# Kernel tuning notes

Measured on AMD Instinct MI355X. Metric: run time of the kernel, lower is better.

Reference implementation:

```python
import jax, jax.numpy as jnp
from jax import lax
import numpy as np

NUM_BLOCK, NUM_LAYER = 4, 10
DILATIONS = [2 ** (i % NUM_LAYER) for i in range(NUM_BLOCK * NUM_LAYER)]


def setup_inputs() -> dict:
    key = jax.random.key(0)
    ks = jax.random.split(key, 6)
    s = 0.05
    return {
        "x": jax.random.normal(ks[0], (8, 256, 16000), dtype=jnp.float32),
        "W_start": jax.random.normal(ks[1], (32, 256), dtype=jnp.float32) * s,
        "W_dil": jax.random.normal(ks[2], (40, 128, 32, 2), dtype=jnp.float32) * s,
        "W_res": jax.random.normal(ks[3], (40, 32, 128), dtype=jnp.float32) * s,
        "W_e1": jax.random.normal(ks[4], (256, 32), dtype=jnp.float32) * s,
        "W_e2": jax.random.normal(ks[5], (256, 256), dtype=jnp.float32) * s,
    }


def _causal_dilated_conv(x, w, dilation):
    # x: [B, Cin, T], w: [Cout, Cin, K=2]. Left-pad (K-1)*dilation -> causal,
    # equivalent to torch symmetric-pad-then-trim-right.
    pad = (w.shape[-1] - 1) * dilation
    return lax.conv_general_dilated(
        x, w, window_strides=(1,), padding=[(pad, 0)],
        rhs_dilation=(dilation,), dimension_numbers=("NCH", "OIH", "NCH"))


def reference(x, W_start, W_dil, W_res, W_e1, W_e2):
    # start 1x1 conv (no bias)
    residual = jnp.einsum("oc,bct->bot", W_start, x)  # [B,32,T]
    skips = jnp.zeros_like(residual)
    for i, d in enumerate(DILATIONS):
        h = _causal_dilated_conv(residual, W_dil[i], d)       # [B,128,T]
        g = jnp.tanh(h) * jax.nn.sigmoid(h)                   # gated activation
        skip = jnp.einsum("oc,bct->bot", W_res[i], g)         # 1x1 -> [B,32,T]
        residual = residual + skip
        skips = skips + skip
    h = jax.nn.relu(skips)
    h = jax.nn.relu(jnp.einsum("oc,bct->bot", W_e1, h))       # [B,256,T]
    logits = jnp.einsum("oc,bct->bot", W_e2, h)               # [B,256,T]
    return logits
```

## Files before the change

### kernel.cpp

```cpp
#include <hip/hip_runtime.h>
#include <math.h>

#define T_LEN 16000
#define NTILE 250
#define TT 64
#define NBLK 2000
#define LGRID 500

static const int N_RES = 8 * 32 * T_LEN;

typedef _Float16 half_t;
typedef __attribute__((ext_vector_type(8))) _Float16 halfx8;
typedef __attribute__((ext_vector_type(4))) _Float16 halfx4;
typedef __attribute__((ext_vector_type(16))) float f32x16;
typedef unsigned int uint32;
typedef unsigned short ushort16;

#define MFMA(a, b, c) __builtin_amdgcn_mfma_f32_32x32x16_f16((a), (b), (c), 0, 0, 0)

static __device__ inline uint32 packpair(float a, float b) {
  half_t ha = (half_t)a, hb = (half_t)b;
  return (uint32)__builtin_bit_cast(ushort16, ha) |
         ((uint32)__builtin_bit_cast(ushort16, hb) << 16);
}

__global__ __launch_bounds__(256) void repack_k(
    const float* __restrict__ Wd, const float* __restrict__ Wr,
    const float* __restrict__ Ws, const float* __restrict__ We1,
    const float* __restrict__ We2,
    half_t* __restrict__ WaG, half_t* __restrict__ WrG, float* __restrict__ WsT,
    half_t* __restrict__ We1S, half_t* __restrict__ We2S) {
  int i = blockIdx.x * 256 + threadIdx.x;
  if (i < 40 * 128 * 128) {
    int l = i >> 14, r = i & 16383, o = r >> 7, k = r & 127;
    int kk = k & 63, c = kk >> 1, s = kk & 1;
    float w = Wd[(((l * 128 + o) * 32 + c) << 1) + s];
    half_t w0 = (half_t)w;
    WaG[i] = (k < 64) ? w0 : (half_t)((w - (float)w0) * 2048.f);
  }
  if (i < 40 * 32 * 256) {
    int l = i >> 13, r = i & 8191, o2 = r >> 8, k = r & 255;
    int kk = k & 127;
    int ks = kk >> 4, lh = (kk >> 3) & 1, j = kk & 7;
    int mh = ks >> 2, til = (ks >> 1) & 1, ab = ks & 1;
    int m = mh * 64 + til * 32 + ab * 16 + (j & 3) + ((j >> 2) << 3) + lh * 4;
    float w = Wr[(l * 32 + o2) * 128 + m];
    half_t w0 = (half_t)w;
    WrG[i] = (k < 128) ? w0 : (half_t)((w - (float)w0) * 2048.f);
  }
  if (i < 8192) {
    int c = i >> 5, o = i & 31;
    WsT[i] = Ws[o * 256 + c];
  }
  if (i < 16384) {
    int o = i >> 6, k = i & 63;
    float w = We1[o * 32 + (k & 31)];
    half_t w0 = (half_t)w;
    We1S[i] = (k < 32) ? w0 : (half_t)((w - (float)w0) * 2048.f);
  }
  if (i < 131072) {
    int o = i >> 9, k = i & 511;
    float w = We2[o * 256 + (k & 255)];
    half_t w0 = (half_t)w;
    We2S[i] = (k < 256) ? w0 : (half_t)((w - (float)w0) * 2048.f);
  }
}

__global__ __launch_bounds__(256) void start_k(const float* __restrict__ x,
                                               const float* __restrict__ WsT,
                                               float* __restrict__ res) {
  __shared__ float xs[32][68];
  int b = blockIdx.x / NTILE;
  int t0 = (blockIdx.x % NTILE) * TT;
  int tid = threadIdx.x;
  int o = tid & 31, tg = (tid >> 5) * 8;
  int lr = tid >> 3, lt = (tid & 7) * 8;
  float acc[8];
#pragma unroll
  for (int j = 0; j < 8; ++j) acc[j] = 0.f;
  for (int cc = 0; cc < 8; ++cc) {
    __syncthreads();
    const float* xp = x + ((size_t)b * 256 + cc * 32 + lr) * T_LEN + t0 + lt;
    *(float4*)&xs[lr][lt]     = *(const float4*)xp;
    *(float4*)&xs[lr][lt + 4] = *(const float4*)(xp + 4);
    __syncthreads();
#pragma unroll 4
    for (int c = 0; c < 32; ++c) {
      float w = WsT[(cc * 32 + c) * 32 + o];
      const float* xr = &xs[c][tg];
#pragma unroll
      for (int j = 0; j < 8; ++j) acc[j] += w * xr[j];
    }
  }
  float* rp = res + ((size_t)b * 32 + o) * T_LEN + t0 + tg;
  *(float4*)rp       = make_float4(acc[0], acc[1], acc[2], acc[3]);
  *(float4*)(rp + 4) = make_float4(acc[4], acc[5], acc[6], acc[7]);
}

#define LOAD_TILE(TI, CV, PV)                                              \
  {                                                                        \
    int tl_ = blockIdx.x + (TI) * LGRID;                                   \
    int bb_ = tl_ / NTILE;                                                 \
    int tb_ = (tl_ - bb_ * NTILE) * TT;                                    \
    const float* rip_ = resIn + ((size_t)bb_ * 32 + cth) * T_LEN;          \
    *(float4*)(CV)       = *(const float4*)(rip_ + tb_ + twh);             \
    *(float4*)((CV) + 4) = *(const float4*)(rip_ + tb_ + twh + 4);         \
    int tp_ = tb_ + twh - d;                                               \
    if (tp_ >= 0 && (d & 3) == 0) {                                        \
      *(float4*)(PV)       = *(const float4*)(rip_ + tp_);                 \
      *(float4*)((PV) + 4) = *(const float4*)(rip_ + tp_ + 4);             \
    } else {                                                               \
      _Pragma("unroll")                                                    \
      for (int j_ = 0; j_ < 8; ++j_) {                                     \
        int q_ = tp_ + j_;                                                 \
        (PV)[j_] = (q_ >= 0) ? rip_[q_] : 0.f;                             \
      }                                                                    \
    }                                                                      \
  }

#define TILE_BODY(TI, CV, PV, NCV, NPV, PREF)                                  \
  {                                                                            \
    int tile = blockIdx.x + (TI) * LGRID;                                      \
    int b = tile / NTILE;                                                      \
    int t0 = (tile - b * NTILE) * TT;                                          \
                                             \
    _Pragma("unroll")                                                          \
    for (int j = 0; j < 8; ++j) {                                              \
      int t = twh + j;                                                         \
      int sw = ((t >> 3) & 3) << 5;                                            \
      char* zrow = sm + t * 272;                                               \
      half_t p0 = (half_t)(PV)[j];                                             \
      half_t c0 = (half_t)(CV)[j];                                             \
      float pl = ((PV)[j] - (float)p0) * 2048.f;                               \
      float cl = ((CV)[j] - (float)c0) * 2048.f;                               \
      *(uint32*)(zrow + ((cth * 4) ^ sw))       = packpair((PV)[j], (CV)[j]);  \
      *(uint32*)(zrow + ((cth * 4 + 128) ^ sw)) = packpair(pl, cl);            \
    }                                                                          \
    __syncthreads();                                                           \
       \
    if (PREF) { LOAD_TILE((TI) + 1, NCV, NPV); }                               \
                                      \
    f32x16 hi0{}, hi1{}, lo0{}, lo1{};                                         \
    {                                                                          \
      int colt = nh * 32 + l31;                                                \
      int sw = ((colt >> 3) & 3) << 5;                                         \
      const char* zr = sm + colt * 272;                                        \
      _Pragma("unroll")                                                        \
      for (int ks = 0; ks < 12; ++ks) {                                        \
        int brow = (ks < 4) ? ks * 16                                          \
                            : ((ks < 8) ? (ks & 3) * 16 + 64 : (ks & 3) * 16); \
        halfx8 bf = *(const halfx8*)(zr + ((brow * 2 + lhi * 16) ^ sw));       \
        if (ks < 4) {                                                          \
          hi0 = MFMA(a1h0[ks], bf, hi0);                                       \
          hi1 = MFMA(a1h1[ks], bf, hi1);                                       \
        } else if (ks < 8) {                                                   \
          lo0 = MFMA(a1h0[ks & 3], bf, lo0);                                   \
          lo1 = MFMA(a1h1[ks & 3], bf, lo1);                                   \
        } else {                                                               \
          lo0 = MFMA(a1l0[ks & 3], bf, lo0);                                   \
          lo1 = MFMA(a1l1[ks & 3], bf, lo1);                                   \
        }                                                                      \
      }                                                                        \
    }                                                                          \
                          \
    halfx8 gh0a, gh0b, gl0a, gl0b, gh1a, gh1b, gl1a, gl1b;                     \
    _Pragma("unroll")                                                          \
    for (int r = 0; r < 16; ++r) {                                             \
      float ha = hi0[r] + lo0[r] * (1.f / 2048.f);                             \
      float hb = hi1[r] + lo1[r] * (1.f / 2048.f);                             \
      ha = fmaxf(ha, -30.f);                                                   \
      hb = fmaxf(hb, -30.f);                                                   \
      float ea = __expf(-ha), eb = __expf(-hb);                                \
      float ga = (1.f - ea) * __builtin_amdgcn_rcpf(1.f + ea * ea);            \
      float gb = (1.f - eb) * __builtin_amdgcn_rcpf(1.f + eb * eb);            \
      half_t ga0 = (half_t)ga;                                                 \
      half_t gb0 = (half_t)gb;                                                 \
      half_t ga1 = (half_t)((ga - (float)ga0) * 2048.f);                       \
      half_t gb1 = (half_t)((gb - (float)gb0) * 2048.f);                       \
      if (r < 8) {                                                             \
        gh0a[r] = ga0; gl0a[r] = ga1; gh1a[r] = gb0; gl1a[r] = gb1;            \
      } else {                                                                 \
        gh0b[r - 8] = ga0; gl0b[r - 8] = ga1;                                  \
        gh1b[r - 8] = gb0; gl1b[r - 8] = gb1;                                  \
      }                                                                        \
    }                                                                          \
                         \
    f32x16 shi{}, slo{};                                                       \
    shi = MFMA(wrHi[0], gh0a, shi);                                            \
    shi = MFMA(wrHi[1], gh0b, shi);                                            \
    shi = MFMA(wrHi[2], gh1a, shi);                                            \
    shi = MFMA(wrHi[3], gh1b, shi);                                            \
    slo = MFMA(wrHi[0], gl0a, slo);                                            \
    slo = MFMA(wrHi[1], gl0b, slo);                                            \
    slo = MFMA(wrHi[2], gl1a, slo);                                            \
    slo = MFMA(wrHi[3], gl1b, slo);                                            \
    slo = MFMA(wrLo[0], gh0a, slo);                                            \
    slo = MFMA(wrLo[1], gh0b, slo);                                            \
    slo = MFMA(wrLo[2], gh1a, slo);                                            \
    slo = MFMA(wrLo[3], gh1b, slo);                                            \
    __syncthreads();                      \
    {                                                                          \
      float* skb = (float*)sm + mh * 32 * 68;                                  \
      _Pragma("unroll")                                                        \
      for (int r = 0; r < 16; ++r) {                                           \
        int row = (r & 3) + 8 * (r >> 2) + 4 * lhi;                            \
        skb[row * 68 + nh * 32 + l31] = shi[r] + slo[r] * (1.f / 2048.f);      \
      }                                                                        \
    }                                                                          \
    __syncthreads();                                                           \
                     \
    {                                                                          \
      const float* s0 = (const float*)sm + cth * 68 + twh;                     \
      const float* s1 = s0 + 32 * 68;                                          \
      size_t base = ((size_t)b * 32 + cth) * T_LEN + t0 + twh;                 \
      _Pragma("unroll")                                                        \
      for (int v = 0; v < 8; v += 4) {                                         \
        float4 sa = *(const float4*)(s0 + v);                                  \
        float4 sb = *(const float4*)(s1 + v);                                  \
        float4 o;                                                              \
        o.x = (CV)[v]     + sa.x + sb.x;                                       \
        o.y = (CV)[v + 1] + sa.y + sb.y;                                       \
        o.z = (CV)[v + 2] + sa.z + sb.z;                                       \
        o.w = (CV)[v + 3] + sa.w + sb.w;                                       \
        *(float4*)(resOut + base + v) = o;                                     \
      }                                                                        \
    }                                                                          \
    __syncthreads();       \
  }

__global__ __launch_bounds__(256, 2) void layer_k(const float* __restrict__ resIn,
                                                  float* __restrict__ resOut,
                                                  const half_t* __restrict__ WaL,
                                                  const half_t* __restrict__ WrL,
                                                  int d) {
  __shared__ __align__(16) char sm[17408];
  int tid = threadIdx.x;
  int wave = tid >> 6, lane = tid & 63;
  int l31 = lane & 31, lhi = lane >> 5;
  int mh = wave & 1, nh = wave >> 1;
  int cth = tid >> 3, twh = (tid & 7) * 8;

  halfx8 a1h0[4], a1l0[4], a1h1[4], a1l1[4];
  {
    const half_t* wa = WaL + (mh * 64 + l31) * 128 + lhi * 8;
#pragma unroll
    for (int j = 0; j < 4; ++j) {
      a1h0[j] = *(const halfx8*)(wa + j * 16);
      a1l0[j] = *(const halfx8*)(wa + 64 + j * 16);
      a1h1[j] = *(const halfx8*)(wa + 32 * 128 + j * 16);
      a1l1[j] = *(const halfx8*)(wa + 32 * 128 + 64 + j * 16);
    }
  }
  halfx8 wrHi[4], wrLo[4];
  {
    const half_t* wr = WrL + l31 * 256 + mh * 64 + lhi * 8;
#pragma unroll
    for (int q = 0; q < 4; ++q) {
      wrHi[q] = *(const halfx8*)(wr + q * 16);
      wrLo[q] = *(const halfx8*)(wr + 128 + q * 16);
    }
  }

  float cvA[8], pvA[8], cvB[8], pvB[8];
  LOAD_TILE(0, cvA, pvA);

  TILE_BODY(0, cvA, pvA, cvB, pvB, 1)
  TILE_BODY(1, cvB, pvB, cvA, pvA, 1)
  TILE_BODY(2, cvA, pvA, cvB, pvB, 1)
  TILE_BODY(3, cvB, pvB, cvA, pvA, 0)
}

__global__ __launch_bounds__(512) void end_k(const float* __restrict__ resF,
                                             const float* __restrict__ res0,
                                             const half_t* __restrict__ We1S,
                                             const half_t* __restrict__ We2S,
                                             float* __restrict__ out) {
  __shared__ __align__(16) char sm[75776];
  const int H2T_OFF = 0, H1F_OFF = 0, H1T_OFF = 66560;
  int tid = threadIdx.x;
  int b = blockIdx.x / NTILE;
  int t0 = (blockIdx.x % NTILE) * TT;

  {
    int c = tid >> 4, tt4 = (tid & 15) * 4;
    size_t base = ((size_t)b * 32 + c) * T_LEN + t0 + tt4;
    float4 f = *(const float4*)(resF + base);
    float4 z = *(const float4*)(res0 + base);
    float* h1 = (float*)(sm + H1F_OFF) + c * 68 + tt4;
    h1[0] = fmaxf(f.x - z.x, 0.f);
    h1[1] = fmaxf(f.y - z.y, 0.f);
    h1[2] = fmaxf(f.z - z.z, 0.f);
    h1[3] = fmaxf(f.w - z.w, 0.f);
  }
  __syncthreads();
  {
    int t = tid & 63, cg2 = tid >> 6;
    const float* h1 = (const float*)(sm + H1F_OFF);
    halfx4 hi, lo;
#pragma unroll
    for (int j = 0; j < 4; ++j) {
      float v = h1[(cg2 * 4 + j) * 68 + t];
      half_t h = (half_t)v;
      hi[j] = h;
      lo[j] = (half_t)((v - (float)h) * 2048.f);
    }
    half_t* h1t = (half_t*)(sm + H1T_OFF) + t * 72;
    *(halfx4*)(h1t + cg2 * 4)      = hi;
    *(halfx4*)(h1t + 32 + cg2 * 4) = lo;
  }
  __syncthreads();

  int wave = tid >> 6, lane = tid & 63;
  int l31 = lane & 31, lhi = lane >> 5;

  f32x16 aHi0{}, aHi1{}, aLo0{}, aLo1{};
  {
    const char* h1t = sm + H1T_OFF;
    const half_t* wp = We1S + (wave * 32 + l31) * 64;
#pragma unroll
    for (int ks = 0; ks < 2; ++ks) {
      halfx8 hiA = *(const halfx8*)(wp + ks * 16 + lhi * 8);
      halfx8 loA = *(const halfx8*)(wp + 32 + ks * 16 + lhi * 8);
      const char* br0 = h1t + l31 * 144;
      const char* br1 = h1t + (32 + l31) * 144;
      halfx8 hiB0 = *(const halfx8*)(br0 + (ks * 16 + lhi * 8) * 2);
      halfx8 loB0 = *(const halfx8*)(br0 + (32 + ks * 16 + lhi * 8) * 2);
      halfx8 hiB1 = *(const halfx8*)(br1 + (ks * 16 + lhi * 8) * 2);
      halfx8 loB1 = *(const halfx8*)(br1 + (32 + ks * 16 + lhi * 8) * 2);
      aHi0 = MFMA(hiA, hiB0, aHi0);
      aLo0 = MFMA(hiA, loB0, aLo0);
      aLo0 = MFMA(loA, hiB0, aLo0);
      aHi1 = MFMA(hiA, hiB1, aHi1);
      aLo1 = MFMA(hiA, loB1, aLo1);
      aLo1 = MFMA(loA, hiB1, aLo1);
    }
  }
  {
#pragma unroll
    for (int n = 0; n < 2; ++n) {
      const f32x16& aH = n ? aHi1 : aHi0;
      const f32x16& aL = n ? aLo1 : aLo0;
      int t = n * 32 + l31;
      half_t* row = (half_t*)(sm + H2T_OFF) + t * 520;
#pragma unroll
      for (int g = 0; g < 4; ++g) {
        halfx4 hi, lo;
#pragma unroll
        for (int j = 0; j < 4; ++j) {
          int r = g * 4 + j;
          float v = aH[r] + aL[r] * (1.f / 2048.f);
          v = fmaxf(v, 0.f);
          half_t h = (half_t)v;
          hi[j] = h;
          lo[j] = (half_t)((v - (float)h) * 2048.f);
        }
        int col = wave * 32 + g * 8 + lhi * 4;
        *(halfx4*)(row + col)       = hi;
        *(halfx4*)(row + 256 + col) = lo;
      }
    }
  }
  __syncthreads();

  f32x16 bHi0{}, bHi1{}, bLo0{}, bLo1{};
  {
    const half_t* wp = We2S + (size_t)(wave * 32 + l31) * 512;
    const char* h2t = sm + H2T_OFF;
#pragma unroll 2
    for (int ks = 0; ks < 16; ++ks) {
      halfx8 hiA = *(const halfx8*)(wp + ks * 16 + lhi * 8);
      halfx8 loA = *(const halfx8*)(wp + 256 + ks * 16 + lhi * 8);
      const char* br0 = h2t + l31 * 1040;
      const char* br1 = h2t + (32 + l31) * 1040;
      halfx8 hiB0 = *(const halfx8*)(br0 + (ks * 16 + lhi * 8) * 2);
      halfx8 loB0 = *(const halfx8*)(br0 + (256 + ks * 16 + lhi * 8) * 2);
      halfx8 hiB1 = *(const halfx8*)(br1 + (ks * 16 + lhi * 8) * 2);
      halfx8 loB1 = *(const halfx8*)(br1 + (256 + ks * 16 + lhi * 8) * 2);
      bHi0 = MFMA(hiA, hiB0, bHi0);
      bLo0 = MFMA(hiA, loB0, bLo0);
      bLo0 = MFMA(loA, hiB0, bLo0);
      bHi1 = MFMA(hiA, hiB1, bHi1);
      bLo1 = MFMA(hiA, loB1, bLo1);
      bLo1 = MFMA(loA, hiB1, bLo1);
    }
  }
  {
#pragma unroll
    for (int n = 0; n < 2; ++n) {
      const f32x16& bH = n ? bHi1 : bHi0;
      const f32x16& bL = n ? bLo1 : bLo0;
      int t = t0 + n * 32 + l31;
#pragma unroll
      for (int r = 0; r < 16; ++r) {
        int o = wave * 32 + (r & 3) + 8 * (r >> 2) + 4 * lhi;
        out[((size_t)b * 256 + o) * T_LEN + t] = bH[r] + bL[r] * (1.f / 2048.f);
      }
    }
  }
}

extern "C" void kernel_launch(void* const* d_in, const int* in_sizes, int n_in,
                              void* d_out, int out_size, void* d_ws, size_t ws_size,
                              hipStream_t stream) {
  const float* x   = (const float*)d_in[0];
  const float* Wst = (const float*)d_in[1];
  const float* Wd  = (const float*)d_in[2];
  const float* Wr  = (const float*)d_in[3];
  const float* We1 = (const float*)d_in[4];
  const float* We2 = (const float*)d_in[5];
  float* out = (float*)d_out;
  float* ws = (float*)d_ws;

  float* resA = ws;
  float* resB = resA + N_RES;
  float* resC = resB + N_RES;
  half_t* WaG  = (half_t*)(resC + N_RES);
  half_t* WrG  = WaG + 40 * 16384;
  float*  WsT  = (float*)(WrG + 40 * 8192);
  half_t* We1S = (half_t*)(WsT + 8192);
  half_t* We2S = We1S + 16384;

  repack_k<<<2560, 256, 0, stream>>>(Wd, Wr, Wst, We1, We2, WaG, WrG, WsT, We1S, We2S);
  start_k<<<NBLK, 256, 0, stream>>>(x, WsT, resA);

  const float* rin = resA;
  for (int l = 0; l < 40; ++l) {
    float* rout = (l & 1) ? resC : resB;
    layer_k<<<LGRID, 256, 0, stream>>>(rin, rout, WaG + l * 16384, WrG + l * 8192,
                                       1 << (l % 10));
    rin = rout;
  }
  end_k<<<NBLK, 512, 0, stream>>>(rin, resA, We1S, We2S, out);
}
```

Measured before the change: 1.050 ms.

## Use split-fp16 MFMA in start conv, drop low terms in end_k, restage layer tiles

The start 1x1 conv moves from scalar FP32 FMAs to split hi/lo fp16 MFMA, with the K dimension split across waves and reduced through LDS. In layer_k, the skip buffer gets its own LDS region so the next tile can be staged into shared memory right after the current output, which removes a barrier per tile at the cost of doubled LDS. In end_k, the activation low-part terms are dropped, giving a 2-term split and smaller LDS with higher occupancy, but this reduces precision of the ReLU activations to fp16.

```diff
diff --git a/kernel.cpp b/kernel.cpp
--- a/kernel.cpp
+++ b/kernel.cpp
@@ -28,7 +28,7 @@
     const float* __restrict__ Wd, const float* __restrict__ Wr,
     const float* __restrict__ Ws, const float* __restrict__ We1,
     const float* __restrict__ We2,
-    half_t* __restrict__ WaG, half_t* __restrict__ WrG, float* __restrict__ WsT,
+    half_t* __restrict__ WaG, half_t* __restrict__ WrG, half_t* __restrict__ WsS,
     half_t* __restrict__ We1S, half_t* __restrict__ We2S) {
   int i = blockIdx.x * 256 + threadIdx.x;
   if (i < 40 * 128 * 128) {
@@ -48,9 +48,11 @@
     half_t w0 = (half_t)w;
     WrG[i] = (k < 128) ? w0 : (half_t)((w - (float)w0) * 2048.f);
   }
-  if (i < 8192) {
-    int c = i >> 5, o = i & 31;
-    WsT[i] = Ws[o * 256 + c];
+  if (i < 16384) {
+    int o = i >> 9, k = i & 511, c = k & 255;
+    float w = Ws[o * 256 + c];
+    half_t w0 = (half_t)w;
+    WsS[i] = (k < 256) ? w0 : (half_t)((w - (float)w0) * 2048.f);
   }
   if (i < 16384) {
     int o = i >> 6, k = i & 63;
@@ -66,35 +68,94 @@
   }
 }
 
-__global__ __launch_bounds__(256) void start_k(const float* __restrict__ x,
-                                               const float* __restrict__ WsT,
-                                               float* __restrict__ res) {
-  __shared__ float xs[32][68];
+__global__ __launch_bounds__(256, 2) void start_k(const float* __restrict__ x,
+                                                  const half_t* __restrict__ WsS,
+                                                  float* __restrict__ res) {
+  __shared__ __align__(16) char sm[51200];
+  const int XS_OFF = 0, SKB_OFF = 33792;
+  int tid = threadIdx.x;
+  int wave = tid >> 6, lane = tid & 63;
+  int l31 = lane & 31, lhi = lane >> 5;
+  int nh = wave & 1, kh = wave >> 1;
   int b = blockIdx.x / NTILE;
   int t0 = (blockIdx.x % NTILE) * TT;
-  int tid = threadIdx.x;
-  int o = tid & 31, tg = (tid >> 5) * 8;
-  int lr = tid >> 3, lt = (tid & 7) * 8;
-  float acc[8];
-#pragma unroll
-  for (int j = 0; j < 8; ++j) acc[j] = 0.f;
-  for (int cc = 0; cc < 8; ++cc) {
+  int c2 = tid & 127;
+  int th = (tid >> 7) * 32;
+  const float* xp0 = x + ((size_t)b * 256 + 2 * c2) * T_LEN + t0 + th;
+  const float* xp1 = xp0 + T_LEN;
+
+  f32x16 accH{}, accL{};
+#pragma unroll
+  for (int p = 0; p < 2; ++p) {
+#pragma unroll
+    for (int q = 0; q < 4; ++q) {
+      float u[8], v[8];
+      *(float4*)u       = *(const float4*)(xp0 + q * 8);
+      *(float4*)(u + 4) = *(const float4*)(xp0 + q * 8 + 4);
+      *(float4*)v       = *(const float4*)(xp1 + q * 8);
+      *(float4*)(v + 4) = *(const float4*)(xp1 + q * 8 + 4);
+#pragma unroll
+      for (int j = 0; j < 8; ++j) {
+        int t = th + q * 8 + j;
+        int sw = ((t >> 3) & 3) << 5;
+        uint32 pk;
+        if (p == 0) {
+          pk = packpair(u[j], v[j]);
+        } else {
+          float l0 = (u[j] - (float)(half_t)u[j]) * 2048.f;
+          float l1 = (v[j] - (float)(half_t)v[j]) * 2048.f;
+          pk = packpair(l0, l1);
+        }
+        *(uint32*)(sm + XS_OFF + t * 528 + ((c2 * 4) ^ sw)) = pk;
+      }
+    }
     __syncthreads();
-    const float* xp = x + ((size_t)b * 256 + cc * 32 + lr) * T_LEN + t0 + lt;
-    *(float4*)&xs[lr][lt]     = *(const float4*)xp;
-    *(float4*)&xs[lr][lt + 4] = *(const float4*)(xp + 4);
+    {
+      int colt = nh * 32 + l31;
+      int sw = ((colt >> 3) & 3) << 5;
+      const char* xr = sm + XS_OFF + colt * 528;
+#pragma unroll
+      for (int ks = 0; ks < 8; ++ks) {
+        int kg = kh * 8 + ks;
+        halfx8 bf = *(const halfx8*)(xr + ((kg * 32 + lhi * 16) ^ sw));
+        halfx8 hiA = *(const halfx8*)(WsS + l31 * 512 + kg * 16 + lhi * 8);
+        if (p == 0) {
+          accH = MFMA(hiA, bf, accH);
+          halfx8 loA = *(const halfx8*)(WsS + l31 * 512 + 256 + kg * 16 + lhi * 8);
+          accL = MFMA(loA, bf, accL);
+        } else {
+          accL = MFMA(hiA, bf, accL);
+        }
+      }
+    }
     __syncthreads();
-#pragma unroll 4
-    for (int c = 0; c < 32; ++c) {
-      float w = WsT[(cc * 32 + c) * 32 + o];
-      const float* xr = &xs[c][tg];
-#pragma unroll
-      for (int j = 0; j < 8; ++j) acc[j] += w * xr[j];
-    }
-  }
-  float* rp = res + ((size_t)b * 32 + o) * T_LEN + t0 + tg;
-  *(float4*)rp       = make_float4(acc[0], acc[1], acc[2], acc[3]);
-  *(float4*)(rp + 4) = make_float4(acc[4], acc[5], acc[6], acc[7]);
+  }
+  {
+    float* skb = (float*)(sm + SKB_OFF) + kh * 32 * 68;
+#pragma unroll
+    for (int r = 0; r < 16; ++r) {
+      int row = (r & 3) + 8 * (r >> 2) + 4 * lhi;
+      skb[row * 68 + nh * 32 + l31] = accH[r] + accL[r] * (1.f / 2048.f);
+    }
+  }
+  __syncthreads();
+  {
+    int cth = tid >> 3, twh = (tid & 7) * 8;
+    const float* s0 = (const float*)(sm + SKB_OFF) + cth * 68 + twh;
+    const float* s1 = s0 + 32 * 68;
+    float* rp = res + ((size_t)b * 32 + cth) * T_LEN + t0 + twh;
+#pragma unroll
+    for (int vq = 0; vq < 8; vq += 4) {
+      float4 sa = *(const float4*)(s0 + vq);
+      float4 sb = *(const float4*)(s1 + vq);
+      float4 o;
+      o.x = sa.x + sb.x;
+      o.y = sa.y + sb.y;
+      o.z = sa.z + sb.z;
+      o.w = sa.w + sb.w;
+      *(float4*)(rp + vq) = o;
+    }
+  }
 }
 
 #define LOAD_TILE(TI, CV, PV)                                              \
@@ -118,26 +179,27 @@
     }                                                                      \
   }
 
+#define STAGE_TILE(CV, PV)                                                 \
+  {                                                                        \
+    _Pragma("unroll")                                                      \
+    for (int j = 0; j < 8; ++j) {                                          \
+      int t = twh + j;                                                     \
+      int sw = ((t >> 3) & 3) << 5;                                        \
+      char* zrow = sm + t * 272;                                           \
+      half_t p0 = (half_t)(PV)[j];                                         \
+      half_t c0 = (half_t)(CV)[j];                                         \
+      float pl = ((PV)[j] - (float)p0) * 2048.f;                           \
+      float cl = ((CV)[j] - (float)c0) * 2048.f;                           \
+      *(uint32*)(zrow + ((cth * 4) ^ sw))       = packpair((PV)[j], (CV)[j]); \
+      *(uint32*)(zrow + ((cth * 4 + 128) ^ sw)) = packpair(pl, cl);        \
+    }                                                                      \
+  }
+
 #define TILE_BODY(TI, CV, PV, NCV, NPV, PREF)                                  \
   {                                                                            \
     int tile = blockIdx.x + (TI) * LGRID;                                      \
     int b = tile / NTILE;                                                      \
     int t0 = (tile - b * NTILE) * TT;                                          \
-                                             \
-    _Pragma("unroll")                                                          \
-    for (int j = 0; j < 8; ++j) {                                              \
-      int t = twh + j;                                                         \
-      int sw = ((t >> 3) & 3) << 5;                                            \
-      char* zrow = sm + t * 272;                                               \
-      half_t p0 = (half_t)(PV)[j];                                             \
-      half_t c0 = (half_t)(CV)[j];                                             \
-      float pl = ((PV)[j] - (float)p0) * 2048.f;                               \
-      float cl = ((CV)[j] - (float)c0) * 2048.f;                               \
-      *(uint32*)(zrow + ((cth * 4) ^ sw))       = packpair((PV)[j], (CV)[j]);  \
-      *(uint32*)(zrow + ((cth * 4 + 128) ^ sw)) = packpair(pl, cl);            \
-    }                                                                          \
-    __syncthreads();                                                           \
-       \
     if (PREF) { LOAD_TILE((TI) + 1, NCV, NPV); }                               \
                                       \
     f32x16 hi0{}, hi1{}, lo0{}, lo1{};                                         \
@@ -198,9 +260,9 @@
     slo = MFMA(wrLo[1], gh0b, slo);                                            \
     slo = MFMA(wrLo[2], gh1a, slo);                                            \
     slo = MFMA(wrLo[3], gh1b, slo);                                            \
-    __syncthreads();                      \
+      \
     {                                                                          \
-      float* skb = (float*)sm + mh * 32 * 68;                                  \
+      float* skb = (float*)(sm + SKB_OFF) + mh * 32 * 68;                      \
       _Pragma("unroll")                                                        \
       for (int r = 0; r < 16; ++r) {                                           \
         int row = (r & 3) + 8 * (r >> 2) + 4 * lhi;                            \
@@ -208,9 +270,9 @@
       }                                                                        \
     }                                                                          \
     __syncthreads();                                                           \
-                     \
+                 \
     {                                                                          \
-      const float* s0 = (const float*)sm + cth * 68 + twh;                     \
+      const float* s0 = (const float*)(sm + SKB_OFF) + cth * 68 + twh;         \
       const float* s1 = s0 + 32 * 68;                                          \
       size_t base = ((size_t)b * 32 + cth) * T_LEN + t0 + twh;                 \
       _Pragma("unroll")                                                        \
@@ -225,7 +287,10 @@
         *(float4*)(resOut + base + v) = o;                                     \
       }                                                                        \
     }                                                                          \
-    __syncthreads();       \
+    if (PREF) {                                                                \
+      STAGE_TILE(NCV, NPV)                                                     \
+      __syncthreads();                                                         \
+    }                                                                          \
   }
 
 __global__ __launch_bounds__(256, 2) void layer_k(const float* __restrict__ resIn,
@@ -233,7 +298,8 @@
                                                   const half_t* __restrict__ WaL,
                                                   const half_t* __restrict__ WrL,
                                                   int d) {
-  __shared__ __align__(16) char sm[17408];
+  __shared__ __align__(16) char sm[34816];
+  const int SKB_OFF = 17408;
   int tid = threadIdx.x;
   int wave = tid >> 6, lane = tid & 63;
   int l31 = lane & 31, lhi = lane >> 5;
@@ -263,6 +329,8 @@
 
   float cvA[8], pvA[8], cvB[8], pvB[8];
   LOAD_TILE(0, cvA, pvA);
+  STAGE_TILE(cvA, pvA)
+  __syncthreads();
 
   TILE_BODY(0, cvA, pvA, cvB, pvB, 1)
   TILE_BODY(1, cvB, pvB, cvA, pvA, 1)
@@ -270,13 +338,13 @@
   TILE_BODY(3, cvB, pvB, cvA, pvA, 0)
 }
 
-__global__ __launch_bounds__(512) void end_k(const float* __restrict__ resF,
-                                             const float* __restrict__ res0,
-                                             const half_t* __restrict__ We1S,
-                                             const half_t* __restrict__ We2S,
-                                             float* __restrict__ out) {
-  __shared__ __align__(16) char sm[75776];
-  const int H2T_OFF = 0, H1F_OFF = 0, H1T_OFF = 66560;
+__global__ __launch_bounds__(512, 6) void end_k(const float* __restrict__ resF,
+                                                const float* __restrict__ res0,
+                                                const half_t* __restrict__ We1S,
+                                                const half_t* __restrict__ We2S,
+                                                float* __restrict__ out) {
+  __shared__ __align__(16) char sm[38912];
+  const int H2T_OFF = 0, H1F_OFF = 0, H1T_OFF = 33792;
   int tid = threadIdx.x;
   int b = blockIdx.x / NTILE;
   int t0 = (blockIdx.x % NTILE) * TT;
@@ -296,17 +364,10 @@
   {
     int t = tid & 63, cg2 = tid >> 6;
     const float* h1 = (const float*)(sm + H1F_OFF);
-    halfx4 hi, lo;
-#pragma unroll
-    for (int j = 0; j < 4; ++j) {
-      float v = h1[(cg2 * 4 + j) * 68 + t];
-      half_t h = (half_t)v;
-      hi[j] = h;
-      lo[j] = (half_t)((v - (float)h) * 2048.f);
-    }
-    half_t* h1t = (half_t*)(sm + H1T_OFF) + t * 72;
-    *(halfx4*)(h1t + cg2 * 4)      = hi;
-    *(halfx4*)(h1t + 32 + cg2 * 4) = lo;
+    halfx4 hi;
+#pragma unroll
+    for (int j = 0; j < 4; ++j) hi[j] = (half_t)h1[(cg2 * 4 + j) * 68 + t];
+    *(halfx4*)(sm + H1T_OFF + t * 80 + cg2 * 8) = hi;
   }
   __syncthreads();
 
@@ -321,18 +382,12 @@
     for (int ks = 0; ks < 2; ++ks) {
       halfx8 hiA = *(const halfx8*)(wp + ks * 16 + lhi * 8);
       halfx8 loA = *(const halfx8*)(wp + 32 + ks * 16 + lhi * 8);
-      const char* br0 = h1t + l31 * 144;
-      const char* br1 = h1t + (32 + l31) * 144;
-      halfx8 hiB0 = *(const halfx8*)(br0 + (ks * 16 + lhi * 8) * 2);
-      halfx8 loB0 = *(const halfx8*)(br0 + (32 + ks * 16 + lhi * 8) * 2);
-      halfx8 hiB1 = *(const halfx8*)(br1 + (ks * 16 + lhi * 8) * 2);
-      halfx8 loB1 = *(const halfx8*)(br1 + (32 + ks * 16 + lhi * 8) * 2);
-      aHi0 = MFMA(hiA, hiB0, aHi0);
-      aLo0 = MFMA(hiA, loB0, aLo0);
-      aLo0 = MFMA(loA, hiB0, aLo0);
-      aHi1 = MFMA(hiA, hiB1, aHi1);
-      aLo1 = MFMA(hiA, loB1, aLo1);
-      aLo1 = MFMA(loA, hiB1, aLo1);
+      halfx8 B0 = *(const halfx8*)(h1t + l31 * 80 + (ks * 16 + lhi * 8) * 2);
+      halfx8 B1 = *(const halfx8*)(h1t + (32 + l31) * 80 + (ks * 16 + lhi * 8) * 2);
+      aHi0 = MFMA(hiA, B0, aHi0);
+      aLo0 = MFMA(loA, B0, aLo0);
+      aHi1 = MFMA(hiA, B1, aHi1);
+      aLo1 = MFMA(loA, B1, aLo1);
     }
   }
   {
@@ -341,22 +396,17 @@
       const f32x16& aH = n ? aHi1 : aHi0;
       const f32x16& aL = n ? aLo1 : aLo0;
       int t = n * 32 + l31;
-      half_t* row = (half_t*)(sm + H2T_OFF) + t * 520;
+      half_t* row = (half_t*)(sm + H2T_OFF) + t * 264;
 #pragma unroll
       for (int g = 0; g < 4; ++g) {
-        halfx4 hi, lo;
+        halfx4 hi;
 #pragma unroll
         for (int j = 0; j < 4; ++j) {
           int r = g * 4 + j;
-          float v = aH[r] + aL[r] * (1.f / 2048.f);
-          v = fmaxf(v, 0.f);
-          half_t h = (half_t)v;
-          hi[j] = h;
-          lo[j] = (half_t)((v - (float)h) * 2048.f);
+          float v = fmaxf(aH[r] + aL[r] * (1.f / 2048.f), 0.f);
+          hi[j] = (half_t)v;
         }
-        int col = wave * 32 + g * 8 + lhi * 4;
-        *(halfx4*)(row + col)       = hi;
-        *(halfx4*)(row + 256 + col) = lo;
+        *(halfx4*)(row + wave * 32 + g * 8 + lhi * 4) = hi;
       }
     }
   }
@@ -370,18 +420,12 @@
     for (int ks = 0; ks < 16; ++ks) {
       halfx8 hiA = *(const halfx8*)(wp + ks * 16 + lhi * 8);
       halfx8 loA = *(const halfx8*)(wp + 256 + ks * 16 + lhi * 8);
-      const char* br0 = h2t + l31 * 1040;
-      const char* br1 = h2t + (32 + l31) * 1040;
-      halfx8 hiB0 = *(const halfx8*)(br0 + (ks * 16 + lhi * 8) * 2);
-      halfx8 loB0 = *(const halfx8*)(br0 + (256 + ks * 16 + lhi * 8) * 2);
-      halfx8 hiB1 = *(const halfx8*)(br1 + (ks * 16 + lhi * 8) * 2);
-      halfx8 loB1 = *(const halfx8*)(br1 + (256 + ks * 16 + lhi * 8) * 2);
-      bHi0 = MFMA(hiA, hiB0, bHi0);
-      bLo0 = MFMA(hiA, loB0, bLo0);
-      bLo0 = MFMA(loA, hiB0, bLo0);
-      bHi1 = MFMA(hiA, hiB1, bHi1);
-      bLo1 = MFMA(hiA, loB1, bLo1);
-      bLo1 = MFMA(loA, hiB1, bLo1);
+      halfx8 B0 = *(const halfx8*)(h2t + l31 * 528 + (ks * 16 + lhi * 8) * 2);
+      halfx8 B1 = *(const halfx8*)(h2t + (32 + l31) * 528 + (ks * 16 + lhi * 8) * 2);
+      bHi0 = MFMA(hiA, B0, bHi0);
+      bLo0 = MFMA(loA, B0, bLo0);
+      bHi1 = MFMA(hiA, B1, bHi1);
+      bLo1 = MFMA(loA, B1, bLo1);
     }
   }
   {
@@ -416,12 +460,12 @@
   float* resC = resB + N_RES;
   half_t* WaG  = (half_t*)(resC + N_RES);
   half_t* WrG  = WaG + 40 * 16384;
-  float*  WsT  = (float*)(WrG + 40 * 8192);
-  half_t* We1S = (half_t*)(WsT + 8192);
+  half_t* WsS  = WrG + 40 * 8192;
+  half_t* We1S = WsS + 16384;
   half_t* We2S = We1S + 16384;
 
-  repack_k<<<2560, 256, 0, stream>>>(Wd, Wr, Wst, We1, We2, WaG, WrG, WsT, We1S, We2S);
-  start_k<<<NBLK, 256, 0, stream>>>(x, WsT, resA);
+  repack_k<<<2560, 256, 0, stream>>>(Wd, Wr, Wst, We1, We2, WaG, WrG, WsS, We1S, We2S);
+  start_k<<<NBLK, 256, 0, stream>>>(x, WsS, resA);
 
   const float* rin = resA;
   for (int l = 0; l < 40; ++l) {
```

Measured after the change: 1.097 ms. 4.4% more time.
